# Kernel optimization log

Measured on AMD Instinct MI355X. Metric: run time of the kernel, lower is better.

## Reference

```python
import jax, jax.numpy as jnp
import numpy as np

L, B, D = 8, 16, 1024  # diagram depth, batch of diagrams, padded layer width


def setup_inputs() -> dict:
    key = jax.random.key(0)
    k1, k2, k3, k4 = jax.random.split(key, 4)
    x = jax.random.normal(k1, (B, D), dtype=jnp.float32)
    # Per-sample block-diagonal weight matrices, one stack per diagram layer.
    # Scale ~ glorot so activations stay bounded through L layers.
    weights = jax.random.normal(k2, (L, B, D, D), dtype=jnp.float32) * (1.0 / np.sqrt(D))
    biases = jax.random.normal(k3, (L, B, D), dtype=jnp.float32)
    masks = jax.random.randint(k4, (L, B, D), 0, 2, dtype=jnp.int32)
    return {"x": x, "weights": weights, "biases": biases, "masks": masks}


def reference(x, weights, biases, masks):
    # Faithful to NeuralDisCoCirc.call: sequential loop over diagram layers,
    # each layer: out = einsum('bi,bij->bj', h, W) + b; masked ReLU.
    mask_bool = masks.astype(bool)

    def step(h, layer):
        w, b, m = layer  # w: [B, D, D], b/m: [B, D]
        out = jnp.einsum('bi,bij->bj', h, w) + b
        out = jnp.where(m, jax.nn.relu(out), out)
        return out, None

    h, _ = jax.lax.scan(step, x, (weights, biases, mask_bool))
    return h
```

## Files before the change

kernel.cpp:

```cpp
#include <hip/hip_runtime.h>

#define L_ 8
#define B_ 16
#define D_ 1024
#define S_ 32
#define SEG (D_ / S_)

__global__ void layer_partial(const float* __restrict__ h,
                              const float* __restrict__ W,
                              float* __restrict__ partial) {
    const int blk = blockIdx.x;
    const int b = blk / S_;
    const int s = blk % S_;
    const int tid = threadIdx.x;

    __shared__ float hs[SEG];
    if (tid < SEG) hs[tid] = h[b * D_ + s * SEG + tid];
    __syncthreads();

    const float4* __restrict__ W4 =
        (const float4*)(W + (size_t)b * D_ * D_ + (size_t)s * SEG * D_);

    float4 acc = {0.f, 0.f, 0.f, 0.f};
#pragma unroll 8
    for (int i = 0; i < SEG; ++i) {
        const float hv = hs[i];
        const float4 w = W4[i * (D_ / 4) + tid];
        acc.x += hv * w.x;
        acc.y += hv * w.y;
        acc.z += hv * w.z;
        acc.w += hv * w.w;
    }

    float4* P4 = (float4*)(partial + (size_t)s * (B_ * D_) + (size_t)b * D_);
    P4[tid] = acc;
}

__global__ void layer_reduce(const float* __restrict__ partial,
                             const float* __restrict__ bias,
                             const int* __restrict__ mask,
                             float* __restrict__ hout) {
    const int t = blockIdx.x * blockDim.x + threadIdx.x;
    float acc = bias[t];
#pragma unroll
    for (int s = 0; s < S_; ++s) acc += partial[s * (B_ * D_) + t];
    if (mask[t]) acc = fmaxf(acc, 0.f);
    hout[t] = acc;
}

extern "C" void kernel_launch(void* const* d_in, const int* in_sizes, int n_in,
                              void* d_out, int out_size, void* d_ws, size_t ws_size,
                              hipStream_t stream) {
    const float* x  = (const float*)d_in[0];
    const float* W  = (const float*)d_in[1];
    const float* Bs = (const float*)d_in[2];
    const int*   M  = (const int*)d_in[3];
    float* out = (float*)d_out;

    float* partial = (float*)d_ws;
    float* hA = partial + (size_t)S_ * B_ * D_;
    float* hB = hA + (size_t)B_ * D_;

    const float* hin = x;
    for (int l = 0; l < L_; ++l) {
        layer_partial<<<B_ * S_, 256, 0, stream>>>(
            hin, W + (size_t)l * B_ * D_ * D_, partial);
        float* hout = (l == L_ - 1) ? out : ((l & 1) ? hB : hA);
        layer_reduce<<<64, 256, 0, stream>>>(
            partial, Bs + (size_t)l * B_ * D_, M + (size_t)l * B_ * D_, hout);
        hin = hout;
    }
}
```

Baseline: 132.6 us.

## Fuse partial matvec and reduction into one kernel with in-block column tiling

Replaces the two-kernel split-K scheme with a single kernel per layer where each block owns 32 output columns and reduces eight row-groups in shared memory before applying bias and masked ReLU. This removes the partial-sum workspace round trip and halves the number of launches. In exchange, weight loads become scalar 128-byte row fragments with large strides instead of wide float4 contiguous rows, which may lower DRAM efficiency.

```diff
diff --git a/kernel.cpp b/kernel.cpp
--- a/kernel.cpp
+++ b/kernel.cpp
@@ -3,49 +3,53 @@
 #define L_ 8
 #define B_ 16
 #define D_ 1024
-#define S_ 32
-#define SEG (D_ / S_)
+#define JT 32
+#define IG 8
+#define ILEN (D_ / IG)
 
-__global__ void layer_partial(const float* __restrict__ h,
-                              const float* __restrict__ W,
-                              float* __restrict__ partial) {
+__global__ __launch_bounds__(256) void layer_full(
+    const float* __restrict__ h,
+    const float* __restrict__ W,
+    const float* __restrict__ bias,
+    const int*   __restrict__ mask,
+    float* __restrict__ hout)
+{
     const int blk = blockIdx.x;
-    const int b = blk / S_;
-    const int s = blk % S_;
+    const int b   = blk / (D_ / JT);
+    const int jt  = blk % (D_ / JT);
     const int tid = threadIdx.x;
+    const int jl  = tid & 31;
+    const int ig  = tid >> 5;
 
-    __shared__ float hs[SEG];
-    if (tid < SEG) hs[tid] = h[b * D_ + s * SEG + tid];
+    __shared__ float hs[D_];
+    {
+        const float4* h4 = (const float4*)(h + (size_t)b * D_);
+        ((float4*)hs)[tid] = h4[tid];
+    }
     __syncthreads();
 
-    const float4* __restrict__ W4 =
-        (const float4*)(W + (size_t)b * D_ * D_ + (size_t)s * SEG * D_);
+    const float* __restrict__ Wp =
+        W + (size_t)b * D_ * D_ + (size_t)(ig * ILEN) * D_ + jt * JT + jl;
+    const float* __restrict__ hp = hs + ig * ILEN;
 
-    float4 acc = {0.f, 0.f, 0.f, 0.f};
-#pragma unroll 8
-    for (int i = 0; i < SEG; ++i) {
-        const float hv = hs[i];
-        const float4 w = W4[i * (D_ / 4) + tid];
-        acc.x += hv * w.x;
-        acc.y += hv * w.y;
-        acc.z += hv * w.z;
-        acc.w += hv * w.w;
+    float acc = 0.f;
+#pragma unroll 16
+    for (int i = 0; i < ILEN; ++i) {
+        acc += hp[i] * Wp[(size_t)i * D_];
     }
 
-    float4* P4 = (float4*)(partial + (size_t)s * (B_ * D_) + (size_t)b * D_);
-    P4[tid] = acc;
-}
+    __shared__ float red[IG][JT];
+    red[ig][jl] = acc;
+    __syncthreads();
 
-__global__ void layer_reduce(const float* __restrict__ partial,
-                             const float* __restrict__ bias,
-                             const int* __restrict__ mask,
-                             float* __restrict__ hout) {
-    const int t = blockIdx.x * blockDim.x + threadIdx.x;
-    float acc = bias[t];
+    if (tid < JT) {
+        const int t = b * D_ + jt * JT + tid;
+        float s = bias[t];
 #pragma unroll
-    for (int s = 0; s < S_; ++s) acc += partial[s * (B_ * D_) + t];
-    if (mask[t]) acc = fmaxf(acc, 0.f);
-    hout[t] = acc;
+        for (int g = 0; g < IG; ++g) s += red[g][tid];
+        if (mask[t]) s = fmaxf(s, 0.f);
+        hout[t] = s;
+    }
 }
 
 extern "C" void kernel_launch(void* const* d_in, const int* in_sizes, int n_in,
@@ -55,19 +59,19 @@
     const float* W  = (const float*)d_in[1];
     const float* Bs = (const float*)d_in[2];
     const int*   M  = (const int*)d_in[3];
-    float* out = (float*)d_out;
 
-    float* partial = (float*)d_ws;
-    float* hA = partial + (size_t)S_ * B_ * D_;
+    float* hA = (float*)d_ws;
     float* hB = hA + (size_t)B_ * D_;
 
     const float* hin = x;
     for (int l = 0; l < L_; ++l) {
-        layer_partial<<<B_ * S_, 256, 0, stream>>>(
-            hin, W + (size_t)l * B_ * D_ * D_, partial);
-        float* hout = (l == L_ - 1) ? out : ((l & 1) ? hB : hA);
-        layer_reduce<<<64, 256, 0, stream>>>(
-            partial, Bs + (size_t)l * B_ * D_, M + (size_t)l * B_ * D_, hout);
+        float* hout = (l == L_ - 1) ? (float*)d_out : ((l & 1) ? hB : hA);
+        layer_full<<<B_ * (D_ / JT), 256, 0, stream>>>(
+            hin,
+            W  + (size_t)l * B_ * D_ * D_,
+            Bs + (size_t)l * B_ * D_,
+            M  + (size_t)l * B_ * D_,
+            hout);
         hin = hout;
     }
 }
```

Result: faster. 122.4 us (-7.7%).
